# Performance work log

Measured on AMD Instinct MI355X. Metric: run time of the kernel, lower is better.

## Reference

```python
import jax, jax.numpy as jnp
import numpy as np

N = 50000        # num nodes
E = 800000       # num edges (before self-loops)
IN = 256         # in_channels
HID = 32         # hidden_channels per head
HEADS = 8
OUT = 64         # out_channels (layer 2, heads=1)
NEG_SLOPE = 0.2  # PyG GATConv default leaky_relu slope


def setup_inputs() -> dict:
    key = jax.random.key(0)
    ks = jax.random.split(key, 12)
    def rn(k, shape, scale=0.1):
        return jax.random.normal(k, shape, dtype=jnp.float32) * scale
    x = jax.random.normal(ks[0], (N, IN), dtype=jnp.float32)
    edge_index = jax.random.randint(ks[1], (2, E), 0, N, dtype=jnp.int64)
    return {
        "x": x,
        "edge_index": edge_index,
        # GATConv 1: in=256 -> 32 per head, 8 heads, concat
        "W1": rn(ks[2], (IN, HEADS * HID)),
        "att_src1": rn(ks[3], (HEADS, HID)),
        "att_dst1": rn(ks[4], (HEADS, HID)),
        "b1": jnp.zeros((HEADS * HID,), jnp.float32),
        # GATConv 2: in=256 -> 64, 1 head
        "W2": rn(ks[5], (HEADS * HID, OUT)),
        "att_src2": rn(ks[6], (1, OUT)),
        "att_dst2": rn(ks[7], (1, OUT)),
        "b2": jnp.zeros((OUT,), jnp.float32),
    }


def _gat_conv(x, src, dst, W, att_src, att_dst, bias, heads, out_ch):
    """PyG-style GATConv (add_self_loops already applied to src/dst).
    x: [N, F_in]; src/dst: [E']; returns [N, heads*out_ch] (concat)."""
    n = x.shape[0]
    h = (x @ W).reshape(n, heads, out_ch)                     # [N,H,F]
    a_src = jnp.einsum('nhf,hf->nh', h, att_src)              # [N,H]
    a_dst = jnp.einsum('nhf,hf->nh', h, att_dst)
    e = jax.nn.leaky_relu(a_src[src] + a_dst[dst], NEG_SLOPE)  # [E',H]
    # scatter-softmax over incoming edges of each dst node
    m = jax.ops.segment_max(e, dst, num_segments=n)            # [N,H]
    ex = jnp.exp(e - m[dst])
    denom = jax.ops.segment_sum(ex, dst, num_segments=n)       # [N,H]
    alpha = ex / denom[dst]                                    # [E',H]
    msg = alpha[:, :, None] * h[src]                           # [E',H,F]
    out = jax.ops.segment_sum(msg, dst, num_segments=n)        # [N,H,F]
    return out.reshape(n, heads * out_ch) + bias


def reference(x, edge_index, W1, att_src1, att_dst1, b1, W2, att_src2, att_dst2, b2):
    n = x.shape[0]
    loop = jnp.arange(n, dtype=edge_index.dtype)
    src = jnp.concatenate([edge_index[0], loop])  # add self-loops (PyG default)
    dst = jnp.concatenate([edge_index[1], loop])
    h = _gat_conv(x, src, dst, W1, att_src1, att_dst1, b1, HEADS, HID)
    h = jax.nn.relu(h)
    out = _gat_conv(h, src, dst, W2, att_src2, att_dst2, b2, 1, OUT)
    return out
```

## Files before the change

kernel.cpp:

```cpp
#include <hip/hip_runtime.h>
#include <hip/hip_bf16.h>


#define HEADS 8
#define HID 32
#define F1 256
#define F2 64
#define NEG_SLOPE 0.2f
#define CAP 128

typedef __attribute__((ext_vector_type(8))) short bf16x8;
typedef __attribute__((ext_vector_type(4))) float f32x4;
typedef __attribute__((ext_vector_type(8))) unsigned short u16x8;

__device__ __forceinline__ unsigned short f2b(float f) {
    union { float f; unsigned int i; } x; x.f = f;
    unsigned int r = x.i + 0x7fffu + ((x.i >> 16) & 1u);
    return (unsigned short)(r >> 16);
}
__device__ __forceinline__ float b2f(unsigned short u) {
    union { unsigned int i; float f; } x; x.i = ((unsigned int)u) << 16;
    return x.f;
}
__device__ __forceinline__ float leaky(float v) {
    return v > 0.f ? v : NEG_SLOPE * v;
}

__global__ void setup_kernel(const float* __restrict__ W1,
                             const float* __restrict__ W2,
                             unsigned short* __restrict__ W1T,
                             unsigned short* __restrict__ W2T,
                             int* __restrict__ cursor, int Nn) {
    const int i = blockIdx.x * 256 + threadIdx.x;
    if (i < F1 * F1) {
        const int k = i >> 8, n = i & (F1 - 1);
        W1T[(size_t)n * F1 + k] = f2b(W1[i]);
    } else if (i < F1 * F1 + F1 * F2) {
        const int j = i - F1 * F1;
        const int k = j >> 6, n = j & (F2 - 1);
        W2T[(size_t)n * F1 + k] = f2b(W2[j]);
    } else if (i < F1 * F1 + F1 * F2 + Nn) {
        cursor[i - F1 * F1 - F1 * F2] = 0;
    }
}

__global__ void scatter_kernel(const int* __restrict__ ei, int E,
                               int* __restrict__ cursor,
                               int* __restrict__ bucket) {
    const int e = blockIdx.x * blockDim.x + threadIdx.x;
    if (e >= E) return;
    const int d = ei[E + e];
    const int pos = atomicAdd(&cursor[d], 1);
    if (pos < CAP) bucket[(size_t)d * CAP + pos] = ei[e];
}

template<int BN, bool A_FP32, int OUT_MODE>
__global__ __launch_bounds__(256) void mfma_gemm(
        const void* __restrict__ A,
        const unsigned short* __restrict__ BT,
        void* __restrict__ C, int M, int N, int K) {
    constexpr int BM = 128, BK = 32;
    __shared__ unsigned short As[BM * BK];
    __shared__ unsigned short Bs[BN * BK];
    const int tid = threadIdx.x;
    const int wave = tid >> 6, lane = tid & 63;
    const int quad = lane >> 4, l16 = lane & 15;
    const int brow = blockIdx.x * BM;
    const int bcol = blockIdx.y * BN;

    constexpr int MI = (BN == 128) ? 4 : 2;
    constexpr int NJ = 4;
    const int wm = (BN == 128) ? (wave & 1) * 64 : wave * 32;
    const int wn = (BN == 128) ? (wave >> 1) * 64 : 0;

    f32x4 acc[MI][NJ] = {};

    for (int k0 = 0; k0 < K; k0 += BK) {
#pragma unroll
        for (int it = 0; it < (BM * BK) / (256 * 8); ++it) {
            const int idx = it * 256 + tid;
            const int r = idx >> 2;
            const int kk = (idx & 3) * 8;
            const int gr = brow + r;
            if (A_FP32) {
                const float* Af = (const float*)A;
                float4 a0 = make_float4(0.f, 0.f, 0.f, 0.f);
                float4 a1 = make_float4(0.f, 0.f, 0.f, 0.f);
                if (gr < M) {
                    a0 = *(const float4*)&Af[(size_t)gr * K + k0 + kk];
                    a1 = *(const float4*)&Af[(size_t)gr * K + k0 + kk + 4];
                }
                ushort4 lo, hi;
                lo.x = f2b(a0.x); lo.y = f2b(a0.y); lo.z = f2b(a0.z); lo.w = f2b(a0.w);
                hi.x = f2b(a1.x); hi.y = f2b(a1.y); hi.z = f2b(a1.z); hi.w = f2b(a1.w);
                *(ushort4*)&As[r * BK + kk] = lo;
                *(ushort4*)&As[r * BK + kk + 4] = hi;
            } else {
                const unsigned short* Ab = (const unsigned short*)A;
                uint4 v = make_uint4(0u, 0u, 0u, 0u);
                if (gr < M) v = *(const uint4*)&Ab[(size_t)gr * K + k0 + kk];
                *(uint4*)&As[r * BK + kk] = v;
            }
        }
#pragma unroll
        for (int it = 0; it < (BN * BK) / (256 * 8); ++it) {
            const int idx = it * 256 + tid;
            const int r = idx >> 2;
            const int kk = (idx & 3) * 8;
            const uint4 v = *(const uint4*)&BT[(size_t)(bcol + r) * K + k0 + kk];
            *(uint4*)&Bs[r * BK + kk] = v;
        }
        __syncthreads();
        bf16x8 af[MI], bfr[NJ];
#pragma unroll
        for (int i = 0; i < MI; ++i)
            af[i] = *(const bf16x8*)&As[(wm + i * 16 + l16) * BK + quad * 8];
#pragma unroll
        for (int j = 0; j < NJ; ++j)
            bfr[j] = *(const bf16x8*)&Bs[(wn + j * 16 + l16) * BK + quad * 8];
#pragma unroll
        for (int i = 0; i < MI; ++i)
#pragma unroll
            for (int j = 0; j < NJ; ++j)
                acc[i][j] = __builtin_amdgcn_mfma_f32_16x16x32_bf16(
                    af[i], bfr[j], acc[i][j], 0, 0, 0);
        __syncthreads();
    }
#pragma unroll
    for (int i = 0; i < MI; ++i) {
#pragma unroll
        for (int r = 0; r < 4; ++r) {
            const int row = brow + wm + i * 16 + quad * 4 + r;
            if (row >= M) continue;
#pragma unroll
            for (int j = 0; j < NJ; ++j) {
                const int col = bcol + wn + j * 16 + l16;
                const float v = acc[i][j][r];
                if (OUT_MODE == 0) {
                    ((float*)C)[(size_t)row * N + col] = v;
                } else if (OUT_MODE == 1) {
                    ((unsigned short*)C)[(size_t)row * N + col] = f2b(v);
                } else {
                    ((unsigned short*)C)[((size_t)(col >> 5) * M + row) * HID
                                         + (col & 31)] = f2b(v);
                }
            }
        }
    }
}

__global__ void att1_kernel(const unsigned short* __restrict__ h1hm,
                            const float* __restrict__ att_src,
                            const float* __restrict__ att_dst,
                            float* __restrict__ a_src,
                            float* __restrict__ a_dst, int Nn) {
    const int n = blockIdx.x * blockDim.x + threadIdx.x;
    const int h = blockIdx.y;
    if (n >= Nn) return;
    const unsigned short* hp = h1hm + ((size_t)h * Nn + n) * HID;
    const float* as = att_src + h * HID;
    const float* ad = att_dst + h * HID;
    float s = 0.f, d = 0.f;
#pragma unroll
    for (int f = 0; f < HID; ++f) {
        const float v = b2f(hp[f]);
        s += v * as[f];
        d += v * ad[f];
    }
    a_src[(size_t)h * Nn + n] = s;
    a_dst[(size_t)h * Nn + n] = d;
}

__global__ void att2_kernel(const unsigned short* __restrict__ h2b,
                            const float* __restrict__ att_src,
                            const float* __restrict__ att_dst,
                            float* __restrict__ a_src,
                            float* __restrict__ a_dst, int Nn) {
    const int n = blockIdx.x * blockDim.x + threadIdx.x;
    if (n >= Nn) return;
    const unsigned short* hp = h2b + (size_t)n * F2;
    float s = 0.f, d = 0.f;
#pragma unroll
    for (int f = 0; f < F2; ++f) {
        const float v = b2f(hp[f]);
        s += v * att_src[f];
        d += v * att_dst[f];
    }
    a_src[n] = s;
    a_dst[n] = d;
}

__global__ __launch_bounds__(256) void gather1_kernel(
        const int* __restrict__ cursor, const int* __restrict__ bucket,
        const float* __restrict__ a_src, const float* __restrict__ a_dst,
        const unsigned short* __restrict__ h1hm, const float* __restrict__ b1,
        unsigned short* __restrict__ out1b, int Nn) {
    const int h = blockIdx.x & 7;
    const int lane = threadIdx.x & 63;
    const int wv = threadIdx.x >> 6;
    const int sub = lane >> 2;
    const int cl  = lane & 3;
    const int d = (blockIdx.x >> 3) * 64 + wv * 16 + sub;
    if (d >= Nn) return;

    const unsigned short* hh = h1hm + (size_t)h * Nn * HID;
    const float* asrc = a_src + (size_t)h * Nn;
    const float adst = a_dst[(size_t)h * Nn + d];

    float denom, acc[8];
    {
        const float w = __expf(leaky(asrc[d] + adst));
        const u16x8 v = *(const u16x8*)&hh[(size_t)d * HID + cl * 8];
        denom = w;
#pragma unroll
        for (int q = 0; q < 8; ++q) acc[q] = w * b2f(v[q]);
    }
    const int base = d * CAP;
    const int cnt = min(cursor[d], CAP);
    for (int i = 0; i < cnt; i += 4) {
        const int4 s4 = *(const int4*)&bucket[base + i];
        int s[4];
        bool ok[4];
        s[0] = s4.x; s[1] = s4.y; s[2] = s4.z; s[3] = s4.w;
#pragma unroll
        for (int j = 0; j < 4; ++j) {
            ok[j] = (i + j) < cnt;
            s[j] = ok[j] ? s[j] : d;
        }
        float e[4];
#pragma unroll
        for (int j = 0; j < 4; ++j) e[j] = asrc[s[j]];
        u16x8 vv[4];
#pragma unroll
        for (int j = 0; j < 4; ++j)
            vv[j] = *(const u16x8*)&hh[(size_t)s[j] * HID + cl * 8];
#pragma unroll
        for (int j = 0; j < 4; ++j) {
            float w = __expf(leaky(e[j] + adst));
            w = ok[j] ? w : 0.f;
            denom += w;
#pragma unroll
            for (int q = 0; q < 8; ++q) acc[q] += w * b2f(vv[j][q]);
        }
    }
    const float inv = 1.f / denom;
    const int c = h * HID + cl * 8;
    u16x8 o;
#pragma unroll
    for (int q = 0; q < 8; ++q)
        o[q] = f2b(fmaxf(acc[q] * inv + b1[c + q], 0.f));
    *(u16x8*)&out1b[(size_t)d * F1 + c] = o;
}

__global__ __launch_bounds__(256) void gather2_kernel(
        const int* __restrict__ cursor, const int* __restrict__ bucket,
        const float* __restrict__ a_src, const float* __restrict__ a_dst,
        const unsigned short* __restrict__ h2b, const float* __restrict__ b2,
        float* __restrict__ out, int Nn) {
    const int lane = threadIdx.x & 63;
    const int sub  = lane >> 4;
    const int l    = lane & 15;
    int d = blockIdx.x * 16 + (threadIdx.x >> 6) * 4 + sub;
    const bool valid = d < Nn;
    if (!valid) d = Nn - 1;
    const int c = l * 4;

    const float adst = a_dst[d];
    float a0, a1, a2, a3, denom;
    {
        const float w = __expf(leaky(a_src[d] + adst));
        const ushort4 v = *(const ushort4*)&h2b[(size_t)d * F2 + c];
        denom = w;
        a0 = w * b2f(v.x); a1 = w * b2f(v.y);
        a2 = w * b2f(v.z); a3 = w * b2f(v.w);
    }
    const int base = d * CAP;
    const int cnt = min(cursor[d], CAP);
    for (int i = 0; i < cnt; i += 4) {
        const int4 s4 = *(const int4*)&bucket[base + i];
        int s[4] = { s4.x, s4.y, s4.z, s4.w };
        float e[4];
        ushort4 vv[4];
#pragma unroll
        for (int jj = 0; jj < 4; ++jj) {
            const bool ok = (i + jj) < cnt;
            const int ss = ok ? s[jj] : d;
            s[jj] = ok ? 1 : -1;
            e[jj] = a_src[ss];
            vv[jj] = *(const ushort4*)&h2b[(size_t)ss * F2 + c];
        }
#pragma unroll
        for (int jj = 0; jj < 4; ++jj) {
            float w = __expf(leaky(e[jj] + adst));
            w = s[jj] < 0 ? 0.f : w;
            denom += w;
            a0 += w * b2f(vv[jj].x); a1 += w * b2f(vv[jj].y);
            a2 += w * b2f(vv[jj].z); a3 += w * b2f(vv[jj].w);
        }
    }
    if (valid) {
        const float inv = 1.f / denom;
        float4 o;
        o.x = a0 * inv + b2[c + 0];
        o.y = a1 * inv + b2[c + 1];
        o.z = a2 * inv + b2[c + 2];
        o.w = a3 * inv + b2[c + 3];
        *(float4*)&out[(size_t)d * F2 + c] = o;
    }
}

extern "C" void kernel_launch(void* const* d_in, const int* in_sizes, int n_in,
                              void* d_out, int out_size, void* d_ws, size_t ws_size,
                              hipStream_t stream) {
    const float* x        = (const float*)d_in[0];
    const int*   ei       = (const int*)d_in[1];
    const float* W1       = (const float*)d_in[2];
    const float* att_src1 = (const float*)d_in[3];
    const float* att_dst1 = (const float*)d_in[4];
    const float* b1       = (const float*)d_in[5];
    const float* W2       = (const float*)d_in[6];
    const float* att_src2 = (const float*)d_in[7];
    const float* att_dst2 = (const float*)d_in[8];
    const float* b2       = (const float*)d_in[9];
    float* out = (float*)d_out;

    const int Nn = in_sizes[0] / F1;
    const int E  = in_sizes[1] / 2;

    char* p = (char*)d_ws;
    unsigned short* h1hm  = (unsigned short*)p; p += (size_t)Nn * F1 * 2;
    unsigned short* out1b = (unsigned short*)p; p += (size_t)Nn * F1 * 2;
    unsigned short* W1T   = (unsigned short*)p; p += (size_t)F1 * F1 * 2;
    unsigned short* W2T   = (unsigned short*)p; p += (size_t)F2 * F1 * 2;
    unsigned short* h2b   = (unsigned short*)p; p += (size_t)Nn * F2 * 2;
    float* a_src1 = (float*)p; p += (size_t)Nn * HEADS * 4;
    float* a_dst1 = (float*)p; p += (size_t)Nn * HEADS * 4;
    float* a_src2 = (float*)p; p += (size_t)Nn * 4;
    float* a_dst2 = (float*)p; p += (size_t)Nn * 4;
    int* cursor  = (int*)p; p += (size_t)Nn * 4;
    int* bucket  = (int*)p; p += (size_t)Nn * CAP * 4;

    {
        const int total = F1 * F1 + F1 * F2 + Nn;
        setup_kernel<<<(total + 255) / 256, 256, 0, stream>>>(
            W1, W2, W1T, W2T, cursor, Nn);
    }
    scatter_kernel<<<(E + 255) / 256, 256, 0, stream>>>(ei, E, cursor, bucket);

    {
        dim3 grid((Nn + 127) / 128, F1 / 128);
        mfma_gemm<128, true, 2><<<grid, 256, 0, stream>>>(
            x, W1T, h1hm, Nn, F1, F1);
    }
    {
        dim3 grid((Nn + 255) / 256, HEADS);
        att1_kernel<<<grid, 256, 0, stream>>>(
            h1hm, att_src1, att_dst1, a_src1, a_dst1, Nn);
    }
    gather1_kernel<<<((Nn + 63) / 64) * 8, 256, 0, stream>>>(
        cursor, bucket, a_src1, a_dst1, h1hm, b1, out1b, Nn);

    {
        dim3 grid((Nn + 127) / 128, F2 / 64);
        mfma_gemm<64, false, 1><<<grid, 256, 0, stream>>>(
            out1b, W2T, h2b, Nn, F2, F1);
    }
    att2_kernel<<<(Nn + 255) / 256, 256, 0, stream>>>(
        h2b, att_src2, att_dst2, a_src2, a_dst2, Nn);
    gather2_kernel<<<(Nn + 15) / 16, 256, 0, stream>>>(
        cursor, bucket, a_src2, a_dst2, h2b, b2, out, Nn);
}
```

Before: 296.5 us.

## Split each destination's edge list across four lane slots and reduce with shuffles

```diff
diff --git a/kernel.cpp b/kernel.cpp
--- a/kernel.cpp
+++ b/kernel.cpp
@@ -198,17 +198,19 @@
     const int h = blockIdx.x & 7;
     const int lane = threadIdx.x & 63;
     const int wv = threadIdx.x >> 6;
-    const int sub = lane >> 2;
-    const int cl  = lane & 3;
-    const int d = (blockIdx.x >> 3) * 64 + wv * 16 + sub;
-    if (d >= Nn) return;
+    const int sub  = lane >> 4;
+    const int slot = (lane >> 2) & 3;
+    const int cl   = lane & 3;
+    int d = (blockIdx.x >> 3) * 16 + wv * 4 + sub;
+    const bool dvalid = d < Nn;
+    if (!dvalid) d = Nn - 1;
 
     const unsigned short* hh = h1hm + (size_t)h * Nn * HID;
     const float* asrc = a_src + (size_t)h * Nn;
     const float adst = a_dst[(size_t)h * Nn + d];
 
-    float denom, acc[8];
-    {
+    float denom = 0.f, acc[8] = {};
+    if (slot == 0) {
         const float w = __expf(leaky(asrc[d] + adst));
         const u16x8 v = *(const u16x8*)&hh[(size_t)d * HID + cl * 8];
         denom = w;
@@ -217,7 +219,7 @@
     }
     const int base = d * CAP;
     const int cnt = min(cursor[d], CAP);
-    for (int i = 0; i < cnt; i += 4) {
+    for (int i = slot * 4; i < cnt; i += 16) {
         const int4 s4 = *(const int4*)&bucket[base + i];
         int s[4];
         bool ok[4];
@@ -243,13 +245,23 @@
             for (int q = 0; q < 8; ++q) acc[q] += w * b2f(vv[j][q]);
         }
     }
-    const float inv = 1.f / denom;
-    const int c = h * HID + cl * 8;
-    u16x8 o;
-#pragma unroll
-    for (int q = 0; q < 8; ++q)
-        o[q] = f2b(fmaxf(acc[q] * inv + b1[c + q], 0.f));
-    *(u16x8*)&out1b[(size_t)d * F1 + c] = o;
+#pragma unroll
+    for (int q = 0; q < 8; ++q) {
+        acc[q] += __shfl_xor(acc[q], 4, 64);
+        acc[q] += __shfl_xor(acc[q], 8, 64);
+    }
+    denom += __shfl_xor(denom, 4, 64);
+    denom += __shfl_xor(denom, 8, 64);
+
+    if (slot == 0 && dvalid) {
+        const float inv = 1.f / denom;
+        const int c = h * HID + cl * 8;
+        u16x8 o;
+#pragma unroll
+        for (int q = 0; q < 8; ++q)
+            o[q] = f2b(fmaxf(acc[q] * inv + b1[c + q], 0.f));
+        *(u16x8*)&out1b[(size_t)d * F1 + c] = o;
+    }
 }
 
 __global__ __launch_bounds__(256) void gather2_kernel(
@@ -258,16 +270,16 @@
         const unsigned short* __restrict__ h2b, const float* __restrict__ b2,
         float* __restrict__ out, int Nn) {
     const int lane = threadIdx.x & 63;
-    const int sub  = lane >> 4;
+    const int slot = lane >> 4;
     const int l    = lane & 15;
-    int d = blockIdx.x * 16 + (threadIdx.x >> 6) * 4 + sub;
-    const bool valid = d < Nn;
-    if (!valid) d = Nn - 1;
+    int d = blockIdx.x * 4 + (threadIdx.x >> 6);
+    const bool dvalid = d < Nn;
+    if (!dvalid) d = Nn - 1;
     const int c = l * 4;
 
     const float adst = a_dst[d];
-    float a0, a1, a2, a3, denom;
-    {
+    float a0 = 0.f, a1 = 0.f, a2 = 0.f, a3 = 0.f, denom = 0.f;
+    if (slot == 0) {
         const float w = __expf(leaky(a_src[d] + adst));
         const ushort4 v = *(const ushort4*)&h2b[(size_t)d * F2 + c];
         denom = w;
@@ -276,7 +288,7 @@
     }
     const int base = d * CAP;
     const int cnt = min(cursor[d], CAP);
-    for (int i = 0; i < cnt; i += 4) {
+    for (int i = slot * 4; i < cnt; i += 16) {
         const int4 s4 = *(const int4*)&bucket[base + i];
         int s[4] = { s4.x, s4.y, s4.z, s4.w };
         float e[4];
@@ -298,7 +310,14 @@
             a2 += w * b2f(vv[jj].z); a3 += w * b2f(vv[jj].w);
         }
     }
-    if (valid) {
+    a0 += __shfl_xor(a0, 16, 64); a0 += __shfl_xor(a0, 32, 64);
+    a1 += __shfl_xor(a1, 16, 64); a1 += __shfl_xor(a1, 32, 64);
+    a2 += __shfl_xor(a2, 16, 64); a2 += __shfl_xor(a2, 32, 64);
+    a3 += __shfl_xor(a3, 16, 64); a3 += __shfl_xor(a3, 32, 64);
+    denom += __shfl_xor(denom, 16, 64);
+    denom += __shfl_xor(denom, 32, 64);
+
+    if (slot == 0 && dvalid) {
         const float inv = 1.f / denom;
         float4 o;
         o.x = a0 * inv + b2[c + 0];
@@ -357,7 +376,7 @@
         att1_kernel<<<grid, 256, 0, stream>>>(
             h1hm, att_src1, att_dst1, a_src1, a_dst1, Nn);
     }
-    gather1_kernel<<<((Nn + 63) / 64) * 8, 256, 0, stream>>>(
+    gather1_kernel<<<((Nn + 15) / 16) * 8, 256, 0, stream>>>(
         cursor, bucket, a_src1, a_dst1, h1hm, b1, out1b, Nn);
 
     {
@@ -367,6 +386,6 @@
     }
     att2_kernel<<<(Nn + 255) / 256, 256, 0, stream>>>(
         h2b, att_src2, att_dst2, a_src2, a_dst2, Nn);
-    gather2_kernel<<<(Nn + 15) / 16, 256, 0, stream>>>(
+    gather2_kernel<<<(Nn + 3) / 4, 256, 0, stream>>>(
         cursor, bucket, a_src2, a_dst2, h2b, b2, out, Nn);
 }
```

New measurement: 293.0 us. About the same (-1.2%).

## Switch layer-1 features to node-major layout and pad buckets with a sentinel node

Applied to the files above, without the earlier changes.

```diff
diff --git a/kernel.cpp b/kernel.cpp
--- a/kernel.cpp
+++ b/kernel.cpp
@@ -30,17 +30,36 @@
                              const float* __restrict__ W2,
                              unsigned short* __restrict__ W1T,
                              unsigned short* __restrict__ W2T,
-                             int* __restrict__ cursor, int Nn) {
+                             int* __restrict__ cursor,
+                             unsigned short* __restrict__ h1b,
+                             unsigned short* __restrict__ h2b,
+                             float* __restrict__ a_src8,
+                             float* __restrict__ a_src2, int Nn) {
     const int i = blockIdx.x * 256 + threadIdx.x;
-    if (i < F1 * F1) {
+    const int T1 = F1 * F1;
+    const int T2 = T1 + F1 * F2;
+    const int T3 = T2 + Nn;
+    const int T4 = T3 + F1;
+    const int T5 = T4 + F2;
+    const int T6 = T5 + 8;
+    const int T7 = T6 + 1;
+    if (i < T1) {
         const int k = i >> 8, n = i & (F1 - 1);
         W1T[(size_t)n * F1 + k] = f2b(W1[i]);
-    } else if (i < F1 * F1 + F1 * F2) {
-        const int j = i - F1 * F1;
+    } else if (i < T2) {
+        const int j = i - T1;
         const int k = j >> 6, n = j & (F2 - 1);
         W2T[(size_t)n * F1 + k] = f2b(W2[j]);
-    } else if (i < F1 * F1 + F1 * F2 + Nn) {
-        cursor[i - F1 * F1 - F1 * F2] = 0;
+    } else if (i < T3) {
+        cursor[i - T2] = 0;
+    } else if (i < T4) {
+        h1b[(size_t)Nn * F1 + (i - T3)] = 0;
+    } else if (i < T5) {
+        h2b[(size_t)Nn * F2 + (i - T4)] = 0;
+    } else if (i < T6) {
+        a_src8[(size_t)Nn * 8 + (i - T5)] = -1e30f;
+    } else if (i < T7) {
+        a_src2[Nn] = -1e30f;
     }
 }
 
@@ -52,6 +71,15 @@
     const int d = ei[E + e];
     const int pos = atomicAdd(&cursor[d], 1);
     if (pos < CAP) bucket[(size_t)d * CAP + pos] = ei[e];
+}
+
+__global__ void pad_kernel(const int* __restrict__ cursor,
+                           int* __restrict__ bucket, int Nn) {
+    const int d = blockIdx.x * 256 + threadIdx.x;
+    if (d >= Nn) return;
+    const int c0 = min(cursor[d], CAP);
+    const int ce = min((c0 + 3) & ~3, CAP);
+    for (int i = c0; i < ce; ++i) bucket[(size_t)d * CAP + i] = Nn;
 }
 
 template<int BN, bool A_FP32, int OUT_MODE>
@@ -138,37 +166,34 @@
                 const float v = acc[i][j][r];
                 if (OUT_MODE == 0) {
                     ((float*)C)[(size_t)row * N + col] = v;
-                } else if (OUT_MODE == 1) {
+                } else {
                     ((unsigned short*)C)[(size_t)row * N + col] = f2b(v);
-                } else {
-                    ((unsigned short*)C)[((size_t)(col >> 5) * M + row) * HID
-                                         + (col & 31)] = f2b(v);
                 }
             }
         }
     }
 }
 
-__global__ void att1_kernel(const unsigned short* __restrict__ h1hm,
-                            const float* __restrict__ att_src,
-                            const float* __restrict__ att_dst,
-                            float* __restrict__ a_src,
-                            float* __restrict__ a_dst, int Nn) {
-    const int n = blockIdx.x * blockDim.x + threadIdx.x;
-    const int h = blockIdx.y;
+__global__ void att1n_kernel(const unsigned short* __restrict__ h1b,
+                             const float* __restrict__ att_src,
+                             const float* __restrict__ att_dst,
+                             float* __restrict__ a_src8,
+                             float* __restrict__ a_dst8, int Nn) {
+    const int idx = blockIdx.x * 256 + threadIdx.x;
+    const int n = idx >> 3, h = idx & 7;
     if (n >= Nn) return;
-    const unsigned short* hp = h1hm + ((size_t)h * Nn + n) * HID;
+    const unsigned short* hp = h1b + (size_t)n * F1 + h * HID;
     const float* as = att_src + h * HID;
     const float* ad = att_dst + h * HID;
-    float s = 0.f, d = 0.f;
+    float s = 0.f, dd = 0.f;
 #pragma unroll
     for (int f = 0; f < HID; ++f) {
         const float v = b2f(hp[f]);
         s += v * as[f];
-        d += v * ad[f];
-    }
-    a_src[(size_t)h * Nn + n] = s;
-    a_dst[(size_t)h * Nn + n] = d;
+        dd += v * ad[f];
+    }
+    a_src8[(size_t)n * 8 + h] = s;
+    a_dst8[(size_t)n * 8 + h] = dd;
 }
 
 __global__ void att2_kernel(const unsigned short* __restrict__ h2b,
@@ -192,63 +217,61 @@
 
 __global__ __launch_bounds__(256) void gather1_kernel(
         const int* __restrict__ cursor, const int* __restrict__ bucket,
-        const float* __restrict__ a_src, const float* __restrict__ a_dst,
-        const unsigned short* __restrict__ h1hm, const float* __restrict__ b1,
+        const float* __restrict__ a_src8, const float* __restrict__ a_dst8,
+        const unsigned short* __restrict__ h1b, const float* __restrict__ b1,
         unsigned short* __restrict__ out1b, int Nn) {
-    const int h = blockIdx.x & 7;
     const int lane = threadIdx.x & 63;
-    const int wv = threadIdx.x >> 6;
-    const int sub = lane >> 2;
-    const int cl  = lane & 3;
-    const int d = (blockIdx.x >> 3) * 64 + wv * 16 + sub;
+    const int wv   = threadIdx.x >> 6;
+    const int slot = lane >> 5;
+    const int l    = lane & 31;
+    const int hd   = l >> 2;
+    const int d = blockIdx.x * 8 + wv * 2 + slot;
     if (d >= Nn) return;
 
-    const unsigned short* hh = h1hm + (size_t)h * Nn * HID;
-    const float* asrc = a_src + (size_t)h * Nn;
-    const float adst = a_dst[(size_t)h * Nn + d];
+    const float adst = a_dst8[(size_t)d * 8 + hd];
 
     float denom, acc[8];
     {
-        const float w = __expf(leaky(asrc[d] + adst));
-        const u16x8 v = *(const u16x8*)&hh[(size_t)d * HID + cl * 8];
+        const float w = __expf(leaky(a_src8[(size_t)d * 8 + hd] + adst));
+        const u16x8 v = *(const u16x8*)&h1b[(size_t)d * F1 + l * 8];
         denom = w;
 #pragma unroll
         for (int q = 0; q < 8; ++q) acc[q] = w * b2f(v[q]);
     }
     const int base = d * CAP;
     const int cnt = min(cursor[d], CAP);
-    for (int i = 0; i < cnt; i += 4) {
+    const int cntp = (cnt + 3) & ~3;
+    for (int i = 0; i < cntp; i += 4) {
         const int4 s4 = *(const int4*)&bucket[base + i];
-        int s[4];
-        bool ok[4];
-        s[0] = s4.x; s[1] = s4.y; s[2] = s4.z; s[3] = s4.w;
+        int s[4] = { s4.x, s4.y, s4.z, s4.w };
+        float e[4];
+#pragma unroll
+        for (int j = 0; j < 4; ++j) e[j] = a_src8[(size_t)s[j] * 8 + hd];
+        u16x8 vv[4];
+#pragma unroll
+        for (int j = 0; j < 4; ++j)
+            vv[j] = *(const u16x8*)&h1b[(size_t)s[j] * F1 + l * 8];
 #pragma unroll
         for (int j = 0; j < 4; ++j) {
-            ok[j] = (i + j) < cnt;
-            s[j] = ok[j] ? s[j] : d;
-        }
-        float e[4];
-#pragma unroll
-        for (int j = 0; j < 4; ++j) e[j] = asrc[s[j]];
-        u16x8 vv[4];
-#pragma unroll
-        for (int j = 0; j < 4; ++j)
-            vv[j] = *(const u16x8*)&hh[(size_t)s[j] * HID + cl * 8];
-#pragma unroll
-        for (int j = 0; j < 4; ++j) {
-            float w = __expf(leaky(e[j] + adst));
-            w = ok[j] ? w : 0.f;
+            const float w = __expf(leaky(e[j] + adst));
             denom += w;
 #pragma unroll
             for (int q = 0; q < 8; ++q) acc[q] += w * b2f(vv[j][q]);
         }
     }
     const float inv = 1.f / denom;
-    const int c = h * HID + cl * 8;
+    const int c = l * 8;
+    const float4 bv0 = *(const float4*)&b1[c];
+    const float4 bv1 = *(const float4*)&b1[c + 4];
     u16x8 o;
-#pragma unroll
-    for (int q = 0; q < 8; ++q)
-        o[q] = f2b(fmaxf(acc[q] * inv + b1[c + q], 0.f));
+    o[0] = f2b(fmaxf(acc[0] * inv + bv0.x, 0.f));
+    o[1] = f2b(fmaxf(acc[1] * inv + bv0.y, 0.f));
+    o[2] = f2b(fmaxf(acc[2] * inv + bv0.z, 0.f));
+    o[3] = f2b(fmaxf(acc[3] * inv + bv0.w, 0.f));
+    o[4] = f2b(fmaxf(acc[4] * inv + bv1.x, 0.f));
+    o[5] = f2b(fmaxf(acc[5] * inv + bv1.y, 0.f));
+    o[6] = f2b(fmaxf(acc[6] * inv + bv1.z, 0.f));
+    o[7] = f2b(fmaxf(acc[7] * inv + bv1.w, 0.f));
     *(u16x8*)&out1b[(size_t)d * F1 + c] = o;
 }
 
@@ -258,11 +281,10 @@
         const unsigned short* __restrict__ h2b, const float* __restrict__ b2,
         float* __restrict__ out, int Nn) {
     const int lane = threadIdx.x & 63;
-    const int sub  = lane >> 4;
+    const int slot = lane >> 4;
     const int l    = lane & 15;
-    int d = blockIdx.x * 16 + (threadIdx.x >> 6) * 4 + sub;
-    const bool valid = d < Nn;
-    if (!valid) d = Nn - 1;
+    const int d = blockIdx.x * 16 + (threadIdx.x >> 6) * 4 + slot;
+    if (d >= Nn) return;
     const int c = l * 4;
 
     const float adst = a_dst[d];
@@ -276,37 +298,32 @@
     }
     const int base = d * CAP;
     const int cnt = min(cursor[d], CAP);
-    for (int i = 0; i < cnt; i += 4) {
+    const int cntp = (cnt + 3) & ~3;
+    for (int i = 0; i < cntp; i += 4) {
         const int4 s4 = *(const int4*)&bucket[base + i];
         int s[4] = { s4.x, s4.y, s4.z, s4.w };
         float e[4];
         ushort4 vv[4];
 #pragma unroll
         for (int jj = 0; jj < 4; ++jj) {
-            const bool ok = (i + jj) < cnt;
-            const int ss = ok ? s[jj] : d;
-            s[jj] = ok ? 1 : -1;
-            e[jj] = a_src[ss];
-            vv[jj] = *(const ushort4*)&h2b[(size_t)ss * F2 + c];
+            e[jj] = a_src[s[jj]];
+            vv[jj] = *(const ushort4*)&h2b[(size_t)s[jj] * F2 + c];
         }
 #pragma unroll
         for (int jj = 0; jj < 4; ++jj) {
-            float w = __expf(leaky(e[jj] + adst));
-            w = s[jj] < 0 ? 0.f : w;
+            const float w = __expf(leaky(e[jj] + adst));
             denom += w;
             a0 += w * b2f(vv[jj].x); a1 += w * b2f(vv[jj].y);
             a2 += w * b2f(vv[jj].z); a3 += w * b2f(vv[jj].w);
         }
     }
-    if (valid) {
-        const float inv = 1.f / denom;
-        float4 o;
-        o.x = a0 * inv + b2[c + 0];
-        o.y = a1 * inv + b2[c + 1];
-        o.z = a2 * inv + b2[c + 2];
-        o.w = a3 * inv + b2[c + 3];
-        *(float4*)&out[(size_t)d * F2 + c] = o;
-    }
+    const float inv = 1.f / denom;
+    float4 o;
+    o.x = a0 * inv + b2[c + 0];
+    o.y = a1 * inv + b2[c + 1];
+    o.z = a2 * inv + b2[c + 2];
+    o.w = a3 * inv + b2[c + 3];
+    *(float4*)&out[(size_t)d * F2 + c] = o;
 }
 
 extern "C" void kernel_launch(void* const* d_in, const int* in_sizes, int n_in,
@@ -328,37 +345,35 @@
     const int E  = in_sizes[1] / 2;
 
     char* p = (char*)d_ws;
-    unsigned short* h1hm  = (unsigned short*)p; p += (size_t)Nn * F1 * 2;
+    unsigned short* h1b   = (unsigned short*)p; p += (size_t)(Nn + 1) * F1 * 2;
     unsigned short* out1b = (unsigned short*)p; p += (size_t)Nn * F1 * 2;
     unsigned short* W1T   = (unsigned short*)p; p += (size_t)F1 * F1 * 2;
     unsigned short* W2T   = (unsigned short*)p; p += (size_t)F2 * F1 * 2;
-    unsigned short* h2b   = (unsigned short*)p; p += (size_t)Nn * F2 * 2;
-    float* a_src1 = (float*)p; p += (size_t)Nn * HEADS * 4;
-    float* a_dst1 = (float*)p; p += (size_t)Nn * HEADS * 4;
-    float* a_src2 = (float*)p; p += (size_t)Nn * 4;
+    unsigned short* h2b   = (unsigned short*)p; p += (size_t)(Nn + 1) * F2 * 2;
+    float* a_src8 = (float*)p; p += (size_t)(Nn + 1) * 8 * 4;
+    float* a_dst8 = (float*)p; p += (size_t)Nn * 8 * 4;
+    float* a_src2 = (float*)p; p += (size_t)(Nn + 4) * 4;
     float* a_dst2 = (float*)p; p += (size_t)Nn * 4;
     int* cursor  = (int*)p; p += (size_t)Nn * 4;
     int* bucket  = (int*)p; p += (size_t)Nn * CAP * 4;
 
     {
-        const int total = F1 * F1 + F1 * F2 + Nn;
+        const int total = F1 * F1 + F1 * F2 + Nn + F1 + F2 + 8 + 1;
         setup_kernel<<<(total + 255) / 256, 256, 0, stream>>>(
-            W1, W2, W1T, W2T, cursor, Nn);
+            W1, W2, W1T, W2T, cursor, h1b, h2b, a_src8, a_src2, Nn);
     }
     scatter_kernel<<<(E + 255) / 256, 256, 0, stream>>>(ei, E, cursor, bucket);
+    pad_kernel<<<(Nn + 255) / 256, 256, 0, stream>>>(cursor, bucket, Nn);
 
     {
         dim3 grid((Nn + 127) / 128, F1 / 128);
-        mfma_gemm<128, true, 2><<<grid, 256, 0, stream>>>(
-            x, W1T, h1hm, Nn, F1, F1);
-    }
-    {
-        dim3 grid((Nn + 255) / 256, HEADS);
-        att1_kernel<<<grid, 256, 0, stream>>>(
-            h1hm, att_src1, att_dst1, a_src1, a_dst1, Nn);
-    }
-    gather1_kernel<<<((Nn + 63) / 64) * 8, 256, 0, stream>>>(
-        cursor, bucket, a_src1, a_dst1, h1hm, b1, out1b, Nn);
+        mfma_gemm<128, true, 1><<<grid, 256, 0, stream>>>(
+            x, W1T, h1b, Nn, F1, F1);
+    }
+    att1n_kernel<<<(Nn * 8 + 255) / 256, 256, 0, stream>>>(
+        h1b, att_src1, att_dst1, a_src8, a_dst8, Nn);
+    gather1_kernel<<<(Nn + 7) / 8, 256, 0, stream>>>(
+        cursor, bucket, a_src8, a_dst8, h1b, b1, out1b, Nn);
 
     {
         dim3 grid((Nn + 127) / 128, F2 / 64);
```

After: 290.9 us. No clear change (-1.9%).
